# Optimization experiments

Measured on AMD Instinct MI355X. Metric: run time of the kernel, lower is better.

The kernel has to match this reference:

```python
import jax, jax.numpy as jnp
import numpy as np

NUM_PQ = 8
TAU_Q = 1.0
EPS = 1e-12


def setup_inputs() -> dict:
    key = jax.random.key(0)
    k1, k2 = jax.random.split(key)
    z = jax.random.normal(k1, (8, 384, 32, 32), dtype=jnp.float32)
    # xavier_uniform bound for [2048, 384] is ~0.0497; approximate scale with normal init
    C = jax.random.normal(k2, (2048, 384), dtype=jnp.float32) * 0.05
    return {"z": z, "C": C, "it": 0}


def _soft_pq(z, C):
    b, c, h, w = z.shape
    K = NUM_PQ
    d = c // K
    # flatten spatial -> [N, K, d] sub-vectors (torch.split along channel == reshape)
    x = z.transpose(0, 2, 3, 1).reshape(-1, K, d)          # [N, K, d]
    cb = C.reshape(-1, K, d)                               # [M, K, d]
    x2 = jnp.sum(x * x, axis=-1)[:, :, None]               # [N, K, 1]
    c2 = jnp.sum(cb * cb, axis=-1).T[None, :, :]           # [1, K, M]
    xc = jnp.einsum('nkd,mkd->nkm', x, cb)                 # [N, K, M]
    dist = x2 + c2 - 2.0 * xc                              # [N, K, M]
    soft = jax.nn.softmax(-TAU_Q * dist, axis=-1)          # per-book softmax over M
    # soft assignment -> weighted codeword sum, concat over books
    Zq = jnp.einsum('nkm,mkd->nkd', soft, cb).reshape(-1, c)
    # JSD between first/second halves of the batch, per book, averaged over books
    N = soft.shape[0]
    p, q = soft[: N // 2], soft[N // 2 :]
    m = 0.5 * (p + q)
    logm = jnp.log(m + EPS)
    kl_pm = jnp.sum(p * (jnp.log(p + EPS) - logm), axis=-1)   # [N/2, K]
    kl_qm = jnp.sum(q * (jnp.log(q + EPS) - logm), axis=-1)
    # per-book JSD = mean over rows; sum over books / K == mean over both axes
    jsd = jnp.mean(0.5 * (kl_pm + kl_qm))
    z_quantized = Zq.reshape(b, h, w, c).transpose(0, 3, 1, 2)
    return z_quantized, jsd


def reference(z, C, it):
    z_quantized, jsd = _soft_pq(z, C)
    return z_quantized, jsd
```

## Files before the change

kernel.cpp:

```cpp
#include <hip/hip_runtime.h>


typedef __attribute__((ext_vector_type(8))) short short8;
typedef __attribute__((ext_vector_type(4))) float f32x4;

#define Z_BCH   (384*1024)
#define JSD_IDX 3145728

__device__ __forceinline__ f32x4 mfma32(short8 a, short8 b, f32x4 c) {
    return __builtin_amdgcn_mfma_f32_16x16x32_bf16(a, b, c, 0, 0, 0);
}
__device__ __forceinline__ unsigned short f2bf(float x) {
    unsigned u = __float_as_uint(x);
    u += 0x7FFF + ((u >> 16) & 1);
    return (unsigned short)(u >> 16);
}
__device__ __forceinline__ unsigned pk2bf(float a, float b) {
    return (unsigned)f2bf(a) | ((unsigned)f2bf(b) << 16);
}
__device__ __forceinline__ float bf2f(unsigned short h) {
    return __uint_as_float(((unsigned)h) << 16);
}

__global__ __launch_bounds__(512, 4)
void pq_db(const float* __restrict__ Zin, const float* __restrict__ Cb,
           float* __restrict__ Out)
{
    __shared__ __align__(16) unsigned char smem[56864];
    unsigned short* cs  = (unsigned short*)smem;
    unsigned short* ctb = (unsigned short*)(smem + 18432);
    unsigned short* xs  = (unsigned short*)smem;
    float* c2p  = (float*)(smem + 52736);
    float* ztP  = (float*)(smem + 54784);
    float* ttP  = (float*)(smem + 55040);
    float* ztQ  = (float*)(smem + 55296);
    float* ttQ  = (float*)(smem + 55552);
    float* ipzP = (float*)(smem + 55808);
    float* ipzQ = (float*)(smem + 56064);
    float* entP = (float*)(smem + 56320);
    float* entQ = (float*)(smem + 56576);
    float* misc = (float*)(smem + 56832);
    float* obuf = (float*)smem;

    const int tid  = threadIdx.x;
    const int lane = tid & 63;
    const int wv   = tid >> 6;
    const int rg   = wv & 3;
    const int chw  = wv >> 2;
    const int lr   = lane & 15;
    const int lg   = lane >> 4;
    const int pg   = blockIdx.x & 63;
    const int k    = blockIdx.x >> 6;

    unsigned short* plds = (unsigned short*)(smem + 32256 + wv*2560);

    short8 av, on;
#pragma unroll
    for (int i = 0; i < 8; ++i) { av[i] = (short)f2bf((float)lr); on[i] = (short)0x3F80; }
    f32x4 zf4 = {0.f,0.f,0.f,0.f};
    f32x4 dm = mfma32(av, on, zf4);
    f32x4 dr = mfma32(on, av, zf4);
    int mS[4], rS[4];
#pragma unroll
    for (int j = 0; j < 4; ++j) {
        mS[j] = ((int)(dm[j]*0.03125f + 0.5f)) & 15;
        rS[j] = ((int)(dr[j]*0.03125f + 0.5f)) & 15;
    }
    const bool packOK = __all(mS[1] == mS[0]+1 && mS[2] == mS[0]+2 && mS[3] == mS[0]+3
                              && rS[1] == rS[0] && rS[2] == rS[0] && rS[3] == rS[0]);

    for (int i = tid; i < 4608; i += 512) ((unsigned*)smem)[i] = 0u;
    if (tid < 256) ((float*)(smem + 54784))[tid] = 0.f;
    __syncthreads();
    for (int i = tid; i < 6144; i += 512) {
        int row = i & 127, d = i >> 7;
        int n = pg*64 + (row & 63) + ((row & 64) ? 4096 : 0);
        xs[row*72 + d] = f2bf(Zin[(size_t)(n >> 10)*Z_BCH + (k*48 + d)*1024 + (n & 1023)]);
    }
    if (tid < 128) { xs[tid*72 + 48] = 0x3F80; xs[tid*72 + 49] = 0x3F80; }
    __syncthreads();
    short8 xf[2][2];
#pragma unroll
    for (int kh = 0; kh < 2; ++kh) {
        xf[0][kh] = *(const short8*)(xs + (rg*16 + lr)*72 + kh*32 + lg*8);
        xf[1][kh] = *(const short8*)(xs + (64 + rg*16 + lr)*72 + kh*32 + lg*8);
    }
    __syncthreads();

    const int sm = tid & 63, p8 = (tid >> 6) & 3;
    const bool lowHalf = (tid < 256);
    float4 va, vb, vc;

#define LOADREG(m0, doCT) do {                                                \
        if (lowHalf || (doCT)) {                                              \
            const float4* crow = (const float4*)(Cb + (size_t)((m0) + sm)*384 + k*48); \
            va = crow[p8*3+0]; vb = crow[p8*3+1]; vc = crow[p8*3+2];          \
        } } while (0)

#define C2WRITE(b) do {                                                       \
        if (lowHalf) {                                                        \
            float c2 = va.x*va.x + va.y*va.y + va.z*va.z + va.w*va.w          \
                     + vb.x*vb.x + vb.y*vb.y + vb.z*vb.z + vb.w*vb.w          \
                     + vc.x*vc.x + vc.y*vc.y + vc.z*vc.z + vc.w*vc.w;         \
            c2p[(b)*256 + sm*4 + p8] = c2;                                    \
        } } while (0)

#define SWRITE(b, doCT) do {                                                  \
        if (lowHalf) {                                                        \
            unsigned short* rw = cs + (b)*4608 + sm*72 + p8*12;               \
            *(uint2*)(rw)     = make_uint2(pk2bf(va.x,va.y), pk2bf(va.z,va.w)); \
            *(uint2*)(rw + 4) = make_uint2(pk2bf(vb.x,vb.y), pk2bf(vb.z,vb.w)); \
            *(uint2*)(rw + 8) = make_uint2(pk2bf(vc.x,vc.y), pk2bf(vc.z,vc.w)); \
            if (tid < 64) {                                                   \
                float c2 = c2p[(b)*256 + tid*4+0] + c2p[(b)*256 + tid*4+1]    \
                         + c2p[(b)*256 + tid*4+2] + c2p[(b)*256 + tid*4+3];   \
                float mh = -0.5f*c2;                                          \
                unsigned short hi = f2bf(mh);                                 \
                unsigned short lo = f2bf(mh - bf2f(hi));                      \
                *(unsigned*)(cs + (b)*4608 + tid*72 + 48) =                   \
                    (unsigned)hi | ((unsigned)lo << 16);                      \
            }                                                                 \
        } else if (doCT) {                                                    \
            unsigned short* bs = ctb + (b)*3456;                              \
            const int d0 = p8*12;                                             \
            bs[(d0+ 0)*72+sm] = f2bf(va.x);  bs[(d0+ 1)*72+sm] = f2bf(va.y);  \
            bs[(d0+ 2)*72+sm] = f2bf(va.z);  bs[(d0+ 3)*72+sm] = f2bf(va.w);  \
            bs[(d0+ 4)*72+sm] = f2bf(vb.x);  bs[(d0+ 5)*72+sm] = f2bf(vb.y);  \
            bs[(d0+ 6)*72+sm] = f2bf(vb.z);  bs[(d0+ 7)*72+sm] = f2bf(vb.w);  \
            bs[(d0+ 8)*72+sm] = f2bf(vc.x);  bs[(d0+ 9)*72+sm] = f2bf(vc.y);  \
            bs[(d0+10)*72+sm] = f2bf(vc.z);  bs[(d0+11)*72+sm] = f2bf(vc.w);  \
        } } while (0)

    float zp[4]={0,0,0,0}, tp[4]={0,0,0,0}, zq[4]={0,0,0,0}, tq[4]={0,0,0,0};

    LOADREG(0, false); C2WRITE(0);
    __syncthreads();
    SWRITE(0, false);
    LOADREG(64, false); C2WRITE(1);
    __syncthreads();

#pragma unroll 1
    for (int t = 0; t < 32; ++t) {
        if (t < 31) SWRITE((t+1)&1, false);
        if (t < 30) LOADREG((t+2)*64, false);
        const unsigned short* cst = cs + (t&1)*4608;
#pragma unroll
        for (int lmt = 0; lmt < 2; ++lmt) {
            const int mt = chw*2 + lmt;
            short8 a0 = *(const short8*)(cst + (mt*16 + lr)*72 + lg*8);
            short8 a1 = *(const short8*)(cst + (mt*16 + lr)*72 + 32 + lg*8);
            f32x4 accP = {0.f,0.f,0.f,0.f}, accQ = {0.f,0.f,0.f,0.f};
            accP = mfma32(a0, xf[0][0], accP);
            accP = mfma32(a1, xf[0][1], accP);
            accQ = mfma32(a0, xf[1][0], accQ);
            accQ = mfma32(a1, xf[1][1], accQ);
#pragma unroll
            for (int j = 0; j < 4; ++j) {
                float sp = 2.f*accP[j], sq = 2.f*accQ[j];
                float e1 = __expf(sp), e2 = __expf(sq);
                zp[j] += e1; tp[j] = fmaf(e1, sp, tp[j]);
                zq[j] += e2; tq[j] = fmaf(e2, sq, tq[j]);
            }
        }
        if (t < 30) C2WRITE(t&1);
        __syncthreads();
    }

#pragma unroll
    for (int j = 0; j < 4; ++j) {
        int r = rg*16 + rS[j];
        atomicAdd(ztP + r, zp[j]); atomicAdd(ttP + r, tp[j]);
        atomicAdd(ztQ + r, zq[j]); atomicAdd(ttQ + r, tq[j]);
    }
    __syncthreads();
    if (tid < 64) {
        float z1 = ztP[tid], t1 = ttP[tid];
        float z2 = ztQ[tid], t2 = ttQ[tid];
        float i1 = 1.f/z1, i2 = 1.f/z2;
        ipzP[tid] = i1; entP[tid] = t1*i1 - __logf(z1);
        ipzQ[tid] = i2; entQ[tid] = t2*i2 - __logf(z2);
    }
    __syncthreads();
    float izp_s[4], izq_s[4];
#pragma unroll
    for (int j = 0; j < 4; ++j) {
        izp_s[j] = ipzP[rg*16 + rS[j]];
        izq_s[j] = ipzQ[rg*16 + rS[j]];
    }

    f32x4 Op[3], Oq[3];
#pragma unroll
    for (int dt = 0; dt < 3; ++dt) { Op[dt] = (f32x4){0.f,0.f,0.f,0.f}; Oq[dt] = (f32x4){0.f,0.f,0.f,0.f}; }
    float cross = 0.f;

    LOADREG(0, true); C2WRITE(0);
    __syncthreads();
    SWRITE(0, true);
    LOADREG(64, true); C2WRITE(1);
    __syncthreads();

#pragma unroll 1
    for (int t = 0; t < 32; ++t) {
        if (t < 31) SWRITE((t+1)&1, true);
        if (t < 30) LOADREG((t+2)*64, true);
        const unsigned short* cst = cs + (t&1)*4608;
        const unsigned short* ctt = ctb + (t&1)*3456;
#pragma unroll
        for (int lmt = 0; lmt < 2; ++lmt) {
            const int mt = chw*2 + lmt;
            short8 a0 = *(const short8*)(cst + (mt*16 + lr)*72 + lg*8);
            short8 a1 = *(const short8*)(cst + (mt*16 + lr)*72 + 32 + lg*8);
            f32x4 accP = {0.f,0.f,0.f,0.f}, accQ = {0.f,0.f,0.f,0.f};
            accP = mfma32(a0, xf[0][0], accP);
            accP = mfma32(a1, xf[0][1], accP);
            accQ = mfma32(a0, xf[1][0], accQ);
            accQ = mfma32(a1, xf[1][1], accQ);
            float e1a[4], e2a[4];
#pragma unroll
            for (int j = 0; j < 4; ++j) {
                float e1 = __expf(2.f*accP[j]);
                float e2 = __expf(2.f*accQ[j]);
                e1a[j] = e1; e2a[j] = e2;
                float p = e1*izp_s[j], q = e2*izq_s[j];
                float ss = p + q;
                cross = fmaf(ss, __logf(fmaf(0.5f, ss, 1e-12f)), cross);
            }
            if (packOK) {
                *(uint2*)(plds + rS[0]*40        + lmt*16 + mS[0]) =
                    make_uint2(pk2bf(e1a[0], e1a[1]), pk2bf(e1a[2], e1a[3]));
                *(uint2*)(plds + (16 + rS[0])*40 + lmt*16 + mS[0]) =
                    make_uint2(pk2bf(e2a[0], e2a[1]), pk2bf(e2a[2], e2a[3]));
            } else {
#pragma unroll
                for (int j = 0; j < 4; ++j) {
                    plds[rS[j]*40        + lmt*16 + mS[j]] = f2bf(e1a[j]);
                    plds[(16 + rS[j])*40 + lmt*16 + mS[j]] = f2bf(e2a[j]);
                }
            }
        }
        {
            short8 pA = *(const short8*)(plds + lr*40        + lg*8);
            short8 qA = *(const short8*)(plds + (16 + lr)*40 + lg*8);
#pragma unroll
            for (int dt = 0; dt < 3; ++dt) {
                short8 cB = *(const short8*)(ctt + (dt*16 + lr)*72 + chw*32 + lg*8);
                Op[dt] = mfma32(pA, cB, Op[dt]);
                Oq[dt] = mfma32(qA, cB, Oq[dt]);
            }
        }
        if (t < 30) C2WRITE(t&1);
        __syncthreads();
    }

#pragma unroll
    for (int off = 1; off < 64; off <<= 1) cross += __shfl_xor(cross, off);
    if (lane == 0) misc[wv] = cross;

    if (chw == 1) {
#pragma unroll
        for (int dt = 0; dt < 3; ++dt)
#pragma unroll
            for (int j = 0; j < 4; ++j) {
                obuf[(rg*32 +      mS[j])*48 + dt*16 + rS[j]] = Op[dt][j];
                obuf[(rg*32 + 16 + mS[j])*48 + dt*16 + rS[j]] = Oq[dt][j];
            }
    }
    __syncthreads();

    if (tid == 0) {
        float es = 0.f;
        for (int r = 0; r < 64; ++r) es += entP[r] + entQ[r];
        float cr = 0.f;
        for (int w = 0; w < 8; ++w) cr += misc[w];
        atomicAdd(Out + JSD_IDX, (es - cr) * (0.5f/32768.f));
    }

    if (chw == 0) {
#pragma unroll
        for (int dt = 0; dt < 3; ++dt)
#pragma unroll
            for (int j = 0; j < 4; ++j) {
                int xr = mS[j];
                int np = pg*64 + rg*16 + xr;
                int nq = np + 4096;
                int chc = k*48 + dt*16 + rS[j];
                float vP = (Op[dt][j] + obuf[(rg*32 +      xr)*48 + dt*16 + rS[j]]) * ipzP[rg*16 + xr];
                float vQ = (Oq[dt][j] + obuf[(rg*32 + 16 + xr)*48 + dt*16 + rS[j]]) * ipzQ[rg*16 + xr];
                Out[(size_t)(np >> 10)*Z_BCH + (size_t)chc*1024 + (np & 1023)] = vP;
                Out[(size_t)(nq >> 10)*Z_BCH + (size_t)chc*1024 + (nq & 1023)] = vQ;
            }
    }
}

extern "C" void kernel_launch(void* const* d_in, const int* in_sizes, int n_in,
                              void* d_out, int out_size, void* d_ws, size_t ws_size,
                              hipStream_t stream)
{
    const float* z = (const float*)d_in[0];
    const float* C = (const float*)d_in[1];
    float* out = (float*)d_out;

    hipMemsetAsync(out + JSD_IDX, 0, sizeof(float), stream);

    pq_db<<<dim3(512), dim3(512), 0, stream>>>(z, C, out);
}
```

Before: 152.8 us.

## Precompute bf16 codebook tiles and norms in a prep kernel, stream them directly

Adds a prep kernel that converts the codebook into bf16 tiles laid out exactly as the main kernel's shared-memory layout: row-major tiles with the -0.5·||c||^2 hi/lo split already in the padding columns, plus transposed tiles for the second GEMM. The main kernel then copies these tiles into LDS as raw 16-byte vectors. This removes the per-block fp32 loads, bf16 conversion, scattered transposed LDS writes, the c2 partial-sum buffer and one barrier per prologue. Previously all 64 blocks per book repeated that conversion work. The cost is an extra kernel launch and a workspace round-trip.

```diff
diff --git a/kernel.cpp b/kernel.cpp
--- a/kernel.cpp
+++ b/kernel.cpp
@@ -6,6 +6,9 @@
 
 #define Z_BCH   (384*1024)
 #define JSD_IDX 3145728
+#define CS_TILE 9216
+#define CT_TILE 6912
+#define CT_OFF  (8*32*CS_TILE)
 
 __device__ __forceinline__ f32x4 mfma32(short8 a, short8 b, f32x4 c) {
     return __builtin_amdgcn_mfma_f32_16x16x32_bf16(a, b, c, 0, 0, 0);
@@ -22,24 +25,65 @@
     return __uint_as_float(((unsigned)h) << 16);
 }
 
+__global__ __launch_bounds__(256)
+void pq_prep(const float* __restrict__ Cb, unsigned char* __restrict__ ws)
+{
+    const int tid = threadIdx.x;
+    const int k   = blockIdx.x >> 5;
+    const int t   = blockIdx.x & 31;
+    const int sm  = tid & 63, p8 = tid >> 6;
+    const int m   = t*64 + sm;
+
+    unsigned short* csT = (unsigned short*)(ws + (size_t)(k*32 + t)*CS_TILE);
+    unsigned short* ctT = (unsigned short*)(ws + CT_OFF + (size_t)(k*32 + t)*CT_TILE);
+
+    const float4* crow = (const float4*)(Cb + (size_t)m*384 + k*48);
+    float4 va = crow[p8*3+0], vb = crow[p8*3+1], vc = crow[p8*3+2];
+    const int d0 = p8*12;
+    *(uint2*)(csT + sm*72 + d0 + 0) = make_uint2(pk2bf(va.x,va.y), pk2bf(va.z,va.w));
+    *(uint2*)(csT + sm*72 + d0 + 4) = make_uint2(pk2bf(vb.x,vb.y), pk2bf(vb.z,vb.w));
+    *(uint2*)(csT + sm*72 + d0 + 8) = make_uint2(pk2bf(vc.x,vc.y), pk2bf(vc.z,vc.w));
+    ctT[(d0+ 0)*72+sm] = f2bf(va.x);  ctT[(d0+ 1)*72+sm] = f2bf(va.y);
+    ctT[(d0+ 2)*72+sm] = f2bf(va.z);  ctT[(d0+ 3)*72+sm] = f2bf(va.w);
+    ctT[(d0+ 4)*72+sm] = f2bf(vb.x);  ctT[(d0+ 5)*72+sm] = f2bf(vb.y);
+    ctT[(d0+ 6)*72+sm] = f2bf(vb.z);  ctT[(d0+ 7)*72+sm] = f2bf(vb.w);
+    ctT[(d0+ 8)*72+sm] = f2bf(vc.x);  ctT[(d0+ 9)*72+sm] = f2bf(vc.y);
+    ctT[(d0+10)*72+sm] = f2bf(vc.z);  ctT[(d0+11)*72+sm] = f2bf(vc.w);
+    if (tid < 64) {
+        const float4* cr2 = (const float4*)(Cb + (size_t)(t*64 + tid)*384 + k*48);
+        float c2 = 0.f;
+#pragma unroll
+        for (int i = 0; i < 12; ++i) {
+            float4 v = cr2[i];
+            c2 += v.x*v.x + v.y*v.y + v.z*v.z + v.w*v.w;
+        }
+        float mh = -0.5f*c2;
+        unsigned short hi = f2bf(mh);
+        unsigned short lo = f2bf(mh - bf2f(hi));
+        *(uint2*)(csT + tid*72 + 48) = make_uint2((unsigned)hi | ((unsigned)lo << 16), 0u);
+        *(uint2*)(csT + tid*72 + 52) = make_uint2(0u, 0u);
+        *(uint2*)(csT + tid*72 + 56) = make_uint2(0u, 0u);
+        *(uint2*)(csT + tid*72 + 60) = make_uint2(0u, 0u);
+    }
+}
+
 __global__ __launch_bounds__(512, 4)
-void pq_db(const float* __restrict__ Zin, const float* __restrict__ Cb,
+void pq_pc(const float* __restrict__ Zin, const unsigned char* __restrict__ ws,
            float* __restrict__ Out)
 {
-    __shared__ __align__(16) unsigned char smem[56864];
+    __shared__ __align__(16) unsigned char smem[54816];
     unsigned short* cs  = (unsigned short*)smem;
     unsigned short* ctb = (unsigned short*)(smem + 18432);
     unsigned short* xs  = (unsigned short*)smem;
-    float* c2p  = (float*)(smem + 52736);
-    float* ztP  = (float*)(smem + 54784);
-    float* ttP  = (float*)(smem + 55040);
-    float* ztQ  = (float*)(smem + 55296);
-    float* ttQ  = (float*)(smem + 55552);
-    float* ipzP = (float*)(smem + 55808);
-    float* ipzQ = (float*)(smem + 56064);
-    float* entP = (float*)(smem + 56320);
-    float* entQ = (float*)(smem + 56576);
-    float* misc = (float*)(smem + 56832);
+    float* ztP  = (float*)(smem + 52736);
+    float* ttP  = (float*)(smem + 52992);
+    float* ztQ  = (float*)(smem + 53248);
+    float* ttQ  = (float*)(smem + 53504);
+    float* ipzP = (float*)(smem + 53760);
+    float* ipzQ = (float*)(smem + 54016);
+    float* entP = (float*)(smem + 54272);
+    float* entQ = (float*)(smem + 54528);
+    float* misc = (float*)(smem + 54784);
     float* obuf = (float*)smem;
 
     const int tid  = threadIdx.x;
@@ -53,24 +97,26 @@
     const int k    = blockIdx.x >> 6;
 
     unsigned short* plds = (unsigned short*)(smem + 32256 + wv*2560);
+    const unsigned char* csg = ws + (size_t)(k*32)*CS_TILE;
+    const unsigned char* ctg = ws + CT_OFF + (size_t)(k*32)*CT_TILE;
 
     short8 av, on;
 #pragma unroll
     for (int i = 0; i < 8; ++i) { av[i] = (short)f2bf((float)lr); on[i] = (short)0x3F80; }
     f32x4 zf4 = {0.f,0.f,0.f,0.f};
-    f32x4 dm = mfma32(av, on, zf4);
-    f32x4 dr = mfma32(on, av, zf4);
+    f32x4 dmv = mfma32(av, on, zf4);
+    f32x4 drv = mfma32(on, av, zf4);
     int mS[4], rS[4];
 #pragma unroll
     for (int j = 0; j < 4; ++j) {
-        mS[j] = ((int)(dm[j]*0.03125f + 0.5f)) & 15;
-        rS[j] = ((int)(dr[j]*0.03125f + 0.5f)) & 15;
+        mS[j] = ((int)(dmv[j]*0.03125f + 0.5f)) & 15;
+        rS[j] = ((int)(drv[j]*0.03125f + 0.5f)) & 15;
     }
     const bool packOK = __all(mS[1] == mS[0]+1 && mS[2] == mS[0]+2 && mS[3] == mS[0]+3
                               && rS[1] == rS[0] && rS[2] == rS[0] && rS[3] == rS[0]);
 
     for (int i = tid; i < 4608; i += 512) ((unsigned*)smem)[i] = 0u;
-    if (tid < 256) ((float*)(smem + 54784))[tid] = 0.f;
+    if (tid < 256) ((float*)(smem + 52736))[tid] = 0.f;
     __syncthreads();
     for (int i = tid; i < 6144; i += 512) {
         int row = i & 127, d = i >> 7;
@@ -87,62 +133,33 @@
     }
     __syncthreads();
 
-    const int sm = tid & 63, p8 = (tid >> 6) & 3;
-    const bool lowHalf = (tid < 256);
-    float4 va, vb, vc;
-
-#define LOADREG(m0, doCT) do {                                                \
-        if (lowHalf || (doCT)) {                                              \
-            const float4* crow = (const float4*)(Cb + (size_t)((m0) + sm)*384 + k*48); \
-            va = crow[p8*3+0]; vb = crow[p8*3+1]; vc = crow[p8*3+2];          \
-        } } while (0)
-
-#define C2WRITE(b) do {                                                       \
-        if (lowHalf) {                                                        \
-            float c2 = va.x*va.x + va.y*va.y + va.z*va.z + va.w*va.w          \
-                     + vb.x*vb.x + vb.y*vb.y + vb.z*vb.z + vb.w*vb.w          \
-                     + vc.x*vc.x + vc.y*vc.y + vc.z*vc.z + vc.w*vc.w;         \
-            c2p[(b)*256 + sm*4 + p8] = c2;                                    \
-        } } while (0)
+    uint4 r0, r1, r2;
+#define LOADREG(t, doCT) do {                                                 \
+        const unsigned char* _c = csg + (size_t)(t)*CS_TILE;                  \
+        r0 = *(const uint4*)(_c + tid*16);                                    \
+        if (tid < 64) r1 = *(const uint4*)(_c + 8192 + tid*16);               \
+        if ((doCT) && tid < 432)                                              \
+            r2 = *(const uint4*)(ctg + (size_t)(t)*CT_TILE + tid*16);         \
+    } while (0)
 
 #define SWRITE(b, doCT) do {                                                  \
-        if (lowHalf) {                                                        \
-            unsigned short* rw = cs + (b)*4608 + sm*72 + p8*12;               \
-            *(uint2*)(rw)     = make_uint2(pk2bf(va.x,va.y), pk2bf(va.z,va.w)); \
-            *(uint2*)(rw + 4) = make_uint2(pk2bf(vb.x,vb.y), pk2bf(vb.z,vb.w)); \
-            *(uint2*)(rw + 8) = make_uint2(pk2bf(vc.x,vc.y), pk2bf(vc.z,vc.w)); \
-            if (tid < 64) {                                                   \
-                float c2 = c2p[(b)*256 + tid*4+0] + c2p[(b)*256 + tid*4+1]    \
-                         + c2p[(b)*256 + tid*4+2] + c2p[(b)*256 + tid*4+3];   \
-                float mh = -0.5f*c2;                                          \
-                unsigned short hi = f2bf(mh);                                 \
-                unsigned short lo = f2bf(mh - bf2f(hi));                      \
-                *(unsigned*)(cs + (b)*4608 + tid*72 + 48) =                   \
-                    (unsigned)hi | ((unsigned)lo << 16);                      \
-            }                                                                 \
-        } else if (doCT) {                                                    \
-            unsigned short* bs = ctb + (b)*3456;                              \
-            const int d0 = p8*12;                                             \
-            bs[(d0+ 0)*72+sm] = f2bf(va.x);  bs[(d0+ 1)*72+sm] = f2bf(va.y);  \
-            bs[(d0+ 2)*72+sm] = f2bf(va.z);  bs[(d0+ 3)*72+sm] = f2bf(va.w);  \
-            bs[(d0+ 4)*72+sm] = f2bf(vb.x);  bs[(d0+ 5)*72+sm] = f2bf(vb.y);  \
-            bs[(d0+ 6)*72+sm] = f2bf(vb.z);  bs[(d0+ 7)*72+sm] = f2bf(vb.w);  \
-            bs[(d0+ 8)*72+sm] = f2bf(vc.x);  bs[(d0+ 9)*72+sm] = f2bf(vc.y);  \
-            bs[(d0+10)*72+sm] = f2bf(vc.z);  bs[(d0+11)*72+sm] = f2bf(vc.w);  \
-        } } while (0)
+        *(uint4*)(smem + (b)*CS_TILE + tid*16) = r0;                          \
+        if (tid < 64) *(uint4*)(smem + (b)*CS_TILE + 8192 + tid*16) = r1;     \
+        if ((doCT) && tid < 432)                                              \
+            *(uint4*)(smem + 18432 + (b)*CT_TILE + tid*16) = r2;              \
+    } while (0)
 
     float zp[4]={0,0,0,0}, tp[4]={0,0,0,0}, zq[4]={0,0,0,0}, tq[4]={0,0,0,0};
 
-    LOADREG(0, false); C2WRITE(0);
-    __syncthreads();
+    LOADREG(0, false);
     SWRITE(0, false);
-    LOADREG(64, false); C2WRITE(1);
+    LOADREG(1, false);
     __syncthreads();
 
 #pragma unroll 1
     for (int t = 0; t < 32; ++t) {
         if (t < 31) SWRITE((t+1)&1, false);
-        if (t < 30) LOADREG((t+2)*64, false);
+        if (t < 30) LOADREG(t+2, false);
         const unsigned short* cst = cs + (t&1)*4608;
 #pragma unroll
         for (int lmt = 0; lmt < 2; ++lmt) {
@@ -162,7 +179,6 @@
                 zq[j] += e2; tq[j] = fmaf(e2, sq, tq[j]);
             }
         }
-        if (t < 30) C2WRITE(t&1);
         __syncthreads();
     }
 
@@ -193,16 +209,15 @@
     for (int dt = 0; dt < 3; ++dt) { Op[dt] = (f32x4){0.f,0.f,0.f,0.f}; Oq[dt] = (f32x4){0.f,0.f,0.f,0.f}; }
     float cross = 0.f;
 
-    LOADREG(0, true); C2WRITE(0);
-    __syncthreads();
+    LOADREG(0, true);
     SWRITE(0, true);
-    LOADREG(64, true); C2WRITE(1);
+    LOADREG(1, true);
     __syncthreads();
 
 #pragma unroll 1
     for (int t = 0; t < 32; ++t) {
         if (t < 31) SWRITE((t+1)&1, true);
-        if (t < 30) LOADREG((t+2)*64, true);
+        if (t < 30) LOADREG(t+2, true);
         const unsigned short* cst = cs + (t&1)*4608;
         const unsigned short* ctt = ctb + (t&1)*3456;
 #pragma unroll
@@ -248,7 +263,6 @@
                 Oq[dt] = mfma32(qA, cB, Oq[dt]);
             }
         }
-        if (t < 30) C2WRITE(t&1);
         __syncthreads();
     }
 
@@ -302,5 +316,6 @@
 
     hipMemsetAsync(out + JSD_IDX, 0, sizeof(float), stream);
 
-    pq_db<<<dim3(512), dim3(512), 0, stream>>>(z, C, out);
-}
+    pq_prep<<<dim3(256), dim3(256), 0, stream>>>(C, (unsigned char*)d_ws);
+    pq_pc<<<dim3(512), dim3(512), 0, stream>>>(z, (const unsigned char*)d_ws, out);
+}
```

After: 146.6 us. 1.04x faster.
